# Kernel optimization log

Hardware: AMD Instinct MI355X
Metric: run time of the kernel (lower is better)

Reference implementation:

```python
import jax, jax.numpy as jnp
import numpy as np
import math

MIN_NORM = 1e-15
EPS = 1e-7
MAX_NORM = 1e6

N = 100000      # num nodes (aaa)
E = 1600000     # num edges
D_IN = 129      # embedding_num (1 time coord + 128 spatial)
D_OUT = 128     # output1_dim
MAXLEN = 50
B = 4096
NCLASS = 5

# ---------------- Hyperboloid manifold ops (HGCN-style) ----------------

def proj(x, c):
    K = 1. / c
    y = x[..., 1:]
    y_sq = jnp.sum(y * y, axis=-1, keepdims=True)
    x0 = jnp.sqrt(jnp.clip(K + y_sq, EPS))
    return jnp.concatenate([x0, y], axis=-1)

def proj_tan0(u, c):
    # zero out the time coordinate
    return jnp.concatenate([jnp.zeros_like(u[..., :1]), u[..., 1:]], axis=-1)

def expmap0(u, c):
    K = 1. / c
    sqrtK = jnp.sqrt(K)
    x = u[..., 1:]
    xn = jnp.maximum(jnp.linalg.norm(x, axis=-1, keepdims=True), MIN_NORM)
    theta = xn / sqrtK
    first = sqrtK * jnp.cosh(theta)
    rest = sqrtK * jnp.sinh(theta) * x / xn
    return proj(jnp.concatenate([first, rest], axis=-1), c)

def logmap0(x, c):
    K = 1. / c
    sqrtK = jnp.sqrt(K)
    y = x[..., 1:]
    yn = jnp.maximum(jnp.linalg.norm(y, axis=-1, keepdims=True), MIN_NORM)
    theta = jnp.clip(x[..., 0:1] / sqrtK, 1.0 + EPS)
    rest = sqrtK * jnp.arccosh(theta) * y / yn
    return jnp.concatenate([jnp.zeros_like(theta), rest], axis=-1)

def minkowski_dot(x, y):
    return jnp.sum(x * y, axis=-1, keepdims=True) - 2.0 * x[..., 0:1] * y[..., 0:1]

def minkowski_norm(u):
    return jnp.sqrt(jnp.clip(minkowski_dot(u, u), EPS))

def expmap(u, x, c):
    K = 1. / c
    sqrtK = jnp.sqrt(K)
    normu = jnp.minimum(minkowski_norm(u), MAX_NORM)
    theta = jnp.maximum(normu / sqrtK, MIN_NORM)
    result = jnp.cosh(theta) * x + jnp.sinh(theta) * u / theta
    return proj(result, c)

def proj_tan(u, x, c):
    ux = jnp.sum(x[..., 1:] * u[..., 1:], axis=-1, keepdims=True)
    vals0 = ux / jnp.clip(x[..., 0:1], EPS)
    return jnp.concatenate([vals0, u[..., 1:]], axis=-1)

def ptransp0(x, u, c):
    K = 1. / c
    sqrtK = jnp.sqrt(K)
    x0 = x[..., 0:1]
    y = x[..., 1:]
    yn = jnp.maximum(jnp.linalg.norm(y, axis=-1, keepdims=True), MIN_NORM)
    yhat = y / yn
    v = jnp.concatenate([-yn, (sqrtK - x0) * yhat], axis=-1)
    alpha = jnp.sum(yhat * u[..., 1:], axis=-1, keepdims=True) / sqrtK
    return proj_tan(u - alpha * v, x, c)

def mobius_add(x, y, c):
    u = logmap0(y, c)
    v = ptransp0(x, jnp.broadcast_to(u, x.shape), c)
    return expmap(v, x, c)

def mobius_add0(x, y, c):
    # tangent-space addition at the origin
    return expmap0(logmap0(x, c) + logmap0(y, c), c)

def mobius_matvec1(m, x, c):
    return expmap0(logmap0(x, c) @ m, c)

def mobius_matvec0(n, x, c):
    # per-row scalar mobius scaling (n is (N,1))
    return expmap0(n * logmap0(x, c), c)

def hyp_bias_point(b, c):
    return proj(expmap0(proj_tan0(b[None, :], c), c), c)

def gcn_layer(x, w, b, rows, cols, vals, c, n_nodes):
    out = mobius_matvec1(w, x, c)
    out = mobius_add(out, hyp_bias_point(b, c), c)
    out = logmap0(out, c)
    out = jax.ops.segment_sum(vals[:, None] * out[cols], rows, num_segments=n_nodes)
    return proj(expmap0(out, c), c)


def setup_inputs() -> dict:
    key = jax.random.key(0)
    ks = jax.random.split(key, 20)
    def ku(k, shape, fan_in):
        bound = 1.0 / math.sqrt(fan_in)
        return jax.random.uniform(k, shape, jnp.float32, -bound, bound)
    inp = {}
    inp['A1_tensor'] = jax.random.normal(ks[0], (N, D_IN), jnp.float32)
    inp['adj_rows'] = jax.random.randint(ks[1], (E,), 0, N)
    inp['adj_cols'] = jax.random.randint(ks[2], (E,), 0, N)
    inp['adj_vals'] = jax.random.uniform(ks[3], (E,), jnp.float32) * 0.1
    inp['batch_idx'] = jax.random.randint(ks[4], (B, 1, MAXLEN), 0, N)
    inp['raw_c'] = jnp.array([math.log(math.exp(1.0) - 1.0)], jnp.float32)
    inp['n_param'] = jax.random.uniform(ks[5], (N, 1), jnp.float32)
    inp['Lin1'] = ku(ks[6], (D_IN, D_OUT), D_IN)
    inp['Lin1_bias'] = ku(ks[7], (D_OUT,), D_IN)
    inp['gc1_w'] = ku(ks[8], (D_IN, D_OUT), D_IN)
    inp['gc1_b'] = ku(ks[9], (D_OUT,), D_IN)
    inp['gc2_w'] = ku(ks[10], (D_OUT, D_OUT), D_OUT)
    inp['gc2_b'] = ku(ks[11], (D_OUT,), D_OUT)
    inp['weight'] = ku(ks[12], (D_OUT, MAXLEN), D_OUT)
    inp['weight2'] = ku(ks[13], (D_OUT, MAXLEN), D_OUT)
    inp['conv1_w'] = ku(ks[14], (MAXLEN,), MAXLEN)
    inp['conv1_b'] = ku(ks[15], (1,), MAXLEN)
    inp['conv2_w'] = ku(ks[16], (MAXLEN,), MAXLEN)
    inp['conv2_b'] = ku(ks[17], (1,), MAXLEN)
    inp['classifier'] = ku(ks[18], (2 * MAXLEN, NCLASS), 2 * MAXLEN)
    inp['classifier_bias'] = ku(ks[19], (NCLASS,), 2 * MAXLEN)
    return inp


def reference(A1_tensor, adj_rows, adj_cols, adj_vals, batch_idx, raw_c, n_param,
              Lin1, Lin1_bias, gc1_w, gc1_b, gc2_w, gc2_b, weight, weight2,
              conv1_w, conv1_b, conv2_w, conv2_b, classifier, classifier_bias):
    c = jax.nn.softplus(raw_c)[0] + 1e-5
    bi = batch_idx[:, 0, :]                       # (B, L)
    flat = bi.reshape(-1)

    x_tan = proj_tan0(A1_tensor, c)
    a = proj(expmap0(x_tan, c), c)                # (N, D_IN)

    a1 = mobius_matvec1(Lin1, a, c)               # (N, D_OUT)
    a1 = mobius_add(a1, hyp_bias_point(Lin1_bias, c), c)
    a2 = mobius_matvec0(n_param, a1, c)

    x_1 = gcn_layer(a, gc1_w, gc1_b, adj_rows, adj_cols, adj_vals, c, N)
    x_1 = mobius_matvec0(1.0 - n_param, x_1, c)
    x_1 = mobius_add0(x_1, a2, c)
    x_2 = gcn_layer(x_1, gc2_w, gc2_b, adj_rows, adj_cols, adj_vals, c, N)

    # readout branch 1: x_2 gathered on batch indices
    s2 = logmap0(x_2[flat].reshape(bi.shape[0], bi.shape[1], D_OUT), c)  # (B,L,D)
    s2 = jnp.einsum('bld,dt->blt', s2, weight)    # (B, L, MAXLEN)
    s2 = jnp.einsum('blt,l->bt', s2, conv1_w) + conv1_b  # kernel-size-1 conv over channels

    # readout branch 2: a1 gathered on batch indices
    s3 = logmap0(a1[flat].reshape(bi.shape[0], bi.shape[1], D_OUT), c)
    s3 = jnp.einsum('bld,dt->blt', s3, weight2)
    s3 = jnp.einsum('blt,l->bt', s3, conv2_w) + conv2_b

    sel = jnp.concatenate([s2, s3], axis=1)       # (B, 2*MAXLEN)
    pre = sel @ classifier + classifier_bias      # (B, NCLASS)
    return jnp.argmax(pre, axis=-1), sel
```

## Files before the change

kernel.cpp:

```cpp
#include <hip/hip_runtime.h>
#include <math.h>


__device__ __forceinline__ float wsum(float x){
  x += __shfl_xor(x, 32);
  x += __shfl_xor(x, 16);
  x += __shfl_xor(x, 8);
  x += __shfl_xor(x, 4);
  x += __shfl_xor(x, 2);
  x += __shfl_xor(x, 1);
  return x;
}

__device__ __forceinline__ void get_c(const float* rc, float& K, float& sK){
  float c = log1pf(expf(rc[0])) + 1e-5f;
  K  = 1.0f / c;
  sK = sqrtf(K);
}

__device__ __forceinline__ float sinhx_over_x(float x){
  if (x > 1e-3f){
    float e  = __expf(x);
    float em = __builtin_amdgcn_rcpf(e);
    return 0.5f*(e - em) * __builtin_amdgcn_rcpf(x);
  }
  return 1.0f + x*x*(1.0f/6.0f);
}

__device__ __forceinline__ float facosh(float x){
  return __logf(x + sqrtf(fmaxf(fmaf(x, x, -1.0f), 0.0f)));
}

__device__ __forceinline__ unsigned int pack_bf16(float x, float y){
  unsigned int bx = __float_as_uint(x);
  unsigned int by = __float_as_uint(y);
  bx = (bx + 0x7fffu + ((bx >> 16) & 1u)) >> 16;
  by = (by + 0x7fffu + ((by >> 16) & 1u)) & 0xffff0000u;
  return bx | by;
}
__device__ __forceinline__ float bf_lo(unsigned int p){ return __uint_as_float(p << 16); }
__device__ __forceinline__ float bf_hi(unsigned int p){ return __uint_as_float(p & 0xffff0000u); }

__device__ __forceinline__ void chain_scalars(float tt, float tu, float uu,
                                              float K, float sK,
                                              float& At, float& Au){
  float xn  = fmaxf(sqrtf(tt), 1e-15f);
  float th  = xn / sK;
  float f   = sinhx_over_x(th);
  float pn2 = f*f*tt;
  float p0  = sqrtf(fmaxf(K + pn2, 1e-7f));
  float S_yu = f * tu;
  float yn  = fmaxf(sqrtf(pn2), 1e-15f);
  float inv_yn = __builtin_amdgcn_rcpf(yn);
  float alpha = S_yu * inv_yn / sK;
  float coef  = alpha * (sK - p0);
  float cy  = coef * inv_yn;
  float cyf = cy * f;
  float pdw  = S_yu - cy*pn2;
  float spsq = uu - 2.f*cy*S_yu + cy*cy*pn2;
  float w0 = pdw / fmaxf(p0, 1e-7f);
  float md = spsq - w0*w0;
  float normu = fminf(sqrtf(fmaxf(md, 1e-7f)), 1e6f);
  float th2 = fmaxf(normu / sK, 1e-15f);
  float e  = __expf(th2);
  float em = __builtin_amdgcn_rcpf(e);
  float ch = 0.5f*(e + em);
  float g  = (th2 > 1e-3f) ? 0.5f*(e - em)*__builtin_amdgcn_rcpf(th2)
                           : 1.0f + th2*th2*(1.0f/6.0f);
  float rn2 = ch*ch*pn2 + 2.f*ch*g*pdw + g*g*spsq;
  float r0 = sqrtf(fmaxf(K + rn2, 1e-7f));
  float ynf = fmaxf(sqrtf(rn2), 1e-15f);
  float thf = fmaxf(r0/sK, 1.f+1e-7f);
  float rf = sK * facosh(thf) * __builtin_amdgcn_rcpf(ynf);
  At = rf*(ch*f - g*cyf);
  Au = rf*g;
}

__global__ __launch_bounds__(256) void stage_a(const float* __restrict__ A1,
                                               float* __restrict__ L,
                                               int* __restrict__ cnt,
                                               const float* __restrict__ b0,
                                               const float* __restrict__ b1,
                                               const float* __restrict__ b2,
                                               float* __restrict__ uu3, int n){
  size_t i = (size_t)blockIdx.x * 256 + threadIdx.x;
  size_t total = (size_t)n * 128;
  if (i < total){
    size_t row = i >> 7; int j = (int)(i & 127);
    L[i] = A1[row*129 + 1 + j];
  }
  if (i < (size_t)n) cnt[i] = 0;
  if (blockIdx.x == 0 && threadIdx.x < 64){
    int lane = threadIdx.x;
    const float* bs[3] = {b0, b1, b2};
    for (int k = 0; k < 3; ++k){
      float x = lane ? bs[k][2*lane] : 0.0f;
      float y = bs[k][2*lane+1];
      float s = wsum(x*x + y*y);
      if (lane == 0) uu3[k] = s;
    }
  }
}

__global__ __launch_bounds__(256) void gemm_chain(const float* __restrict__ A,
                                                  const float* __restrict__ W,
                                                  const float* __restrict__ bias,
                                                  const float* __restrict__ uu3, int uuidx,
                                                  const float* __restrict__ raw_c,
                                                  float* __restrict__ outF,
                                                  unsigned int* __restrict__ outH,
                                                  int mode, int nrows){
  __shared__ float As[16][132];
  __shared__ float Ws[16][132];
  int tid = threadIdx.x;
  int r0  = blockIdx.x * 128;
  int tx  = tid & 15, ty = tid >> 4;
  float4 aA[2], aW[2];
  int rowA[2], kqA[2], kW[2], cqW[2];
  #pragma unroll
  for (int t = 0; t < 2; ++t){
    int f = tid + t*256;
    rowA[t] = f >> 2; kqA[t] = f & 3;
    kW[t]   = f >> 5; cqW[t] = f & 31;
  }

  auto loadA = [&](int kc){
    #pragma unroll
    for (int t = 0; t < 2; ++t){
      int rg = r0 + rowA[t];
      aA[t] = make_float4(0.f,0.f,0.f,0.f);
      if (rg < nrows) aA[t] = *(const float4*)&A[(size_t)rg*128 + kc*16 + kqA[t]*4];
    }
  };
  auto loadW = [&](int kc){
    #pragma unroll
    for (int t = 0; t < 2; ++t)
      aW[t] = *(const float4*)&W[(size_t)(kc*16 + kW[t])*128 + cqW[t]*4];
  };

  float acc[8][8];
  #pragma unroll
  for (int i = 0; i < 8; ++i)
    #pragma unroll
    for (int j = 0; j < 8; ++j) acc[i][j] = 0.f;

  loadA(0); loadW(0);
  for (int kc = 0; kc < 8; ++kc){
    __syncthreads();
    #pragma unroll
    for (int t = 0; t < 2; ++t){
      As[kqA[t]*4+0][rowA[t]] = aA[t].x;
      As[kqA[t]*4+1][rowA[t]] = aA[t].y;
      As[kqA[t]*4+2][rowA[t]] = aA[t].z;
      As[kqA[t]*4+3][rowA[t]] = aA[t].w;
      *(float4*)&Ws[kW[t]][cqW[t]*4] = aW[t];
    }
    __syncthreads();
    if (kc < 7){ loadA(kc+1); loadW(kc+1); }
    #pragma unroll
    for (int k = 0; k < 16; ++k){
      float4 a0 = *(const float4*)&As[k][ty*8];
      float4 a1 = *(const float4*)&As[k][ty*8+4];
      float4 w0 = *(const float4*)&Ws[k][tx*8];
      float4 w1 = *(const float4*)&Ws[k][tx*8+4];
      float av[8] = {a0.x,a0.y,a0.z,a0.w,a1.x,a1.y,a1.z,a1.w};
      float wv[8] = {w0.x,w0.y,w0.z,w0.w,w1.x,w1.y,w1.z,w1.w};
      #pragma unroll
      for (int i = 0; i < 8; ++i)
        #pragma unroll
        for (int j = 0; j < 8; ++j)
          acc[i][j] = fmaf(av[i], wv[j], acc[i][j]);
    }
  }

  float K, sK; get_c(raw_c, K, sK);
  float uu = uu3[uuidx];
  float uv[8];
  #pragma unroll
  for (int j = 0; j < 8; ++j){
    int col = tx*8 + j;
    uv[j] = (col == 0) ? 0.f : bias[col];
  }
  if (tx == 0){
    #pragma unroll
    for (int i = 0; i < 8; ++i) acc[i][0] = 0.f;
  }
  #pragma unroll
  for (int i = 0; i < 8; ++i){
    float tt = 0.f, tu = 0.f;
    #pragma unroll
    for (int j = 0; j < 8; ++j){
      tt = fmaf(acc[i][j], acc[i][j], tt);
      tu = fmaf(acc[i][j], uv[j], tu);
    }
    #pragma unroll
    for (int m = 1; m <= 8; m <<= 1){
      tt += __shfl_xor(tt, m);
      tu += __shfl_xor(tu, m);
    }
    float At, Au; chain_scalars(tt, tu, uu, K, sK, At, Au);
    int rg = r0 + ty*8 + i;
    if (rg < nrows){
      float o[8];
      #pragma unroll
      for (int j = 0; j < 8; ++j) o[j] = fmaf(At, acc[i][j], Au*uv[j]);
      if (mode == 0){
        *(float4*)&outF[(size_t)rg*128 + tx*8]     = make_float4(o[0],o[1],o[2],o[3]);
        *(float4*)&outF[(size_t)rg*128 + tx*8 + 4] = make_float4(o[4],o[5],o[6],o[7]);
      } else {
        uint4 pk;
        pk.x = pack_bf16(o[0], o[1]);
        pk.y = pack_bf16(o[2], o[3]);
        pk.z = pack_bf16(o[4], o[5]);
        pk.w = pack_bf16(o[6], o[7]);
        *(uint4*)&outH[(size_t)rg*64 + tx*4] = pk;
      }
    }
  }
}

__global__ __launch_bounds__(256) void hist_k(const int* __restrict__ rows,
                                              int* __restrict__ cnt,
                                              int* __restrict__ rnk, int e){
  int base = (blockIdx.x * 256 + threadIdx.x) * 4;
  if (base + 3 < e){
    int4 r = *(const int4*)&rows[base];
    int k0 = atomicAdd(&cnt[r.x], 1);
    int k1 = atomicAdd(&cnt[r.y], 1);
    int k2 = atomicAdd(&cnt[r.z], 1);
    int k3 = atomicAdd(&cnt[r.w], 1);
    *(int4*)&rnk[base] = make_int4(k0, k1, k2, k3);
  } else {
    for (int i = base; i < e; ++i) rnk[i] = atomicAdd(&cnt[rows[i]], 1);
  }
}

#define SCAN_ITEMS 4
__global__ __launch_bounds__(256) void scan1(const int* __restrict__ cnt,
                                             int* __restrict__ off,
                                             int* __restrict__ bsum, int n){
  __shared__ int sh[256];
  int tid = threadIdx.x;
  int base = blockIdx.x * 256 * SCAN_ITEMS + tid * SCAN_ITEMS;
  int v[SCAN_ITEMS]; int s = 0;
  #pragma unroll
  for (int i = 0; i < SCAN_ITEMS; ++i){ int idx = base+i; v[i] = (idx < n) ? cnt[idx] : 0; s += v[i]; }
  sh[tid] = s; __syncthreads();
  for (int o = 1; o < 256; o <<= 1){
    int t = (tid >= o) ? sh[tid - o] : 0; __syncthreads();
    sh[tid] += t; __syncthreads();
  }
  int excl = sh[tid] - s;
  if (tid == 255) bsum[blockIdx.x] = sh[tid];
  int run = excl;
  #pragma unroll
  for (int i = 0; i < SCAN_ITEMS; ++i){ int idx = base+i; if (idx < n) off[idx] = run; run += v[i]; }
}

__global__ void scan2(int* bsum, int G){
  if (threadIdx.x == 0 && blockIdx.x == 0){
    int run = 0;
    for (int i = 0; i < G; ++i){ int t = bsum[i]; bsum[i] = run; run += t; }
  }
}

__global__ void scan3(int* __restrict__ off, const int* __restrict__ bsum, int n){
  int i = blockIdx.x * blockDim.x + threadIdx.x;
  if (i < n) off[i] += bsum[i / (256*SCAN_ITEMS)];
}

__global__ __launch_bounds__(256) void fill_k(const int* __restrict__ rows,
                                              const int* __restrict__ cols,
                                              const float* __restrict__ vals,
                                              const int* __restrict__ off,
                                              const int* __restrict__ rnk,
                                              int2* __restrict__ ecv, int e){
  int base = (blockIdx.x * 256 + threadIdx.x) * 4;
  if (base + 3 < e){
    int4   r = *(const int4*)&rows[base];
    int4   q = *(const int4*)&rnk[base];
    int4   c = *(const int4*)&cols[base];
    float4 v = *(const float4*)&vals[base];
    int o0 = off[r.x], o1 = off[r.y], o2 = off[r.z], o3 = off[r.w];
    ecv[o0 + q.x] = make_int2(c.x, __float_as_int(v.x));
    ecv[o1 + q.y] = make_int2(c.y, __float_as_int(v.y));
    ecv[o2 + q.z] = make_int2(c.z, __float_as_int(v.z));
    ecv[o3 + q.w] = make_int2(c.w, __float_as_int(v.w));
  } else {
    for (int i = base; i < e; ++i)
      ecv[off[rows[i]] + rnk[i]] = make_int2(cols[i], __float_as_int(vals[i]));
  }
}

__device__ __forceinline__ float2 seg_gather_bf16(const unsigned int* __restrict__ h,
                                                  const int* __restrict__ off,
                                                  const int* __restrict__ cnt,
                                                  const int2* __restrict__ ecv,
                                                  int row, int lane){
  float ax = 0.f, ay = 0.f, bx = 0.f, by = 0.f;
  int st = off[row], deg = cnt[row];
  const unsigned int* __restrict__ hb = h + lane;
  for (int b = 0; b < deg; b += 64){
    int k = b + lane;
    int cc = 0; float vv = 0.f;
    if (k < deg){ int2 e = ecv[st+k]; cc = e.x; vv = __int_as_float(e.y); }
    int m = min(64, deg - b);
    for (int j = 0; j < m; j += 8){
      int   c0=__shfl(cc,j+0), c1=__shfl(cc,j+1), c2=__shfl(cc,j+2), c3=__shfl(cc,j+3);
      int   c4=__shfl(cc,j+4), c5=__shfl(cc,j+5), c6=__shfl(cc,j+6), c7=__shfl(cc,j+7);
      float v0=__shfl(vv,j+0), v1=__shfl(vv,j+1), v2=__shfl(vv,j+2), v3=__shfl(vv,j+3);
      float v4=__shfl(vv,j+4), v5=__shfl(vv,j+5), v6=__shfl(vv,j+6), v7=__shfl(vv,j+7);
      unsigned int p0 = hb[(size_t)c0*64];
      unsigned int p1 = hb[(size_t)c1*64];
      unsigned int p2 = hb[(size_t)c2*64];
      unsigned int p3 = hb[(size_t)c3*64];
      unsigned int p4 = hb[(size_t)c4*64];
      unsigned int p5 = hb[(size_t)c5*64];
      unsigned int p6 = hb[(size_t)c6*64];
      unsigned int p7 = hb[(size_t)c7*64];
      ax = fmaf(v0, bf_lo(p0), ax); ay = fmaf(v0, bf_hi(p0), ay);
      bx = fmaf(v1, bf_lo(p1), bx); by = fmaf(v1, bf_hi(p1), by);
      ax = fmaf(v2, bf_lo(p2), ax); ay = fmaf(v2, bf_hi(p2), ay);
      bx = fmaf(v3, bf_lo(p3), bx); by = fmaf(v3, bf_hi(p3), by);
      ax = fmaf(v4, bf_lo(p4), ax); ay = fmaf(v4, bf_hi(p4), ay);
      bx = fmaf(v5, bf_lo(p5), bx); by = fmaf(v5, bf_hi(p5), by);
      ax = fmaf(v6, bf_lo(p6), ax); ay = fmaf(v6, bf_hi(p6), ay);
      bx = fmaf(v7, bf_lo(p7), bx); by = fmaf(v7, bf_hi(p7), by);
    }
  }
  return make_float2(ax + bx, ay + by);
}

__global__ __launch_bounds__(256) void seg_x1(const unsigned int* __restrict__ h1,
                                              const int* __restrict__ off,
                                              const int* __restrict__ cnt,
                                              const int2* __restrict__ ecv,
                                              const float* __restrict__ loga1,
                                              const float* __restrict__ nparam,
                                              float* __restrict__ Lx1, int n){
  int row  = (int)((blockIdx.x * blockDim.x + threadIdx.x) >> 6);
  int lane = threadIdx.x & 63;
  if (row >= n) return;
  float2 acc = seg_gather_bf16(h1, off, cnt, ecv, row, lane);
  float nv = nparam[row];
  float2 la1 = *(const float2*)&loga1[(size_t)row*128 + 2*lane];
  float ox = (1.f-nv)*acc.x + nv*la1.x;
  float oy = (1.f-nv)*acc.y + nv*la1.y;
  *(float2*)&Lx1[(size_t)row*128 + 2*lane] = make_float2(ox, oy);
}

__global__ __launch_bounds__(256) void seg_x2(const unsigned int* __restrict__ h2,
                                              const int* __restrict__ off,
                                              const int* __restrict__ cnt,
                                              const int2* __restrict__ ecv,
                                              float* __restrict__ Lx2, int n){
  int row  = (int)((blockIdx.x * blockDim.x + threadIdx.x) >> 6);
  int lane = threadIdx.x & 63;
  if (row >= n) return;
  float2 acc = seg_gather_bf16(h2, off, cnt, ecv, row, lane);
  *(float2*)&Lx2[(size_t)row*128 + 2*lane] = acc;
}

__global__ __launch_bounds__(128) void batch_head(const float* __restrict__ Lx2,
                                                  const float* __restrict__ loga1,
                                                  const int* __restrict__ bidx,
                                                  const float* __restrict__ weight,
                                                  const float* __restrict__ weight2,
                                                  const float* __restrict__ c1w,
                                                  const float* __restrict__ c1b,
                                                  const float* __restrict__ c2w,
                                                  const float* __restrict__ c2b,
                                                  const float* __restrict__ cls,
                                                  const float* __restrict__ clsb,
                                                  float* __restrict__ out, int Bn){
  __shared__ float sg2[128], sg3[128], ssel[100], spre[5];
  __shared__ int sbi[50];
  __shared__ float sc1[50], sc2[50];
  int b = blockIdx.x, d = threadIdx.x;
  const int* bi = bidx + (size_t)b * 50;
  if (d < 50){ sbi[d] = bi[d]; sc1[d] = c1w[d]; sc2[d] = c2w[d]; }
  __syncthreads();
  int lane = d & 63;
  bool lo = d < 64;
  const float* __restrict__ tab = lo ? Lx2 : loga1;
  const float* __restrict__ cw = lo ? sc1 : sc2;
  float gx = 0.f, gy = 0.f;
  const float2* __restrict__ t2 = (const float2*)tab + lane;
  #pragma unroll
  for (int l = 0; l < 50; l += 5){
    int i0 = sbi[l+0], i1 = sbi[l+1], i2 = sbi[l+2], i3 = sbi[l+3], i4 = sbi[l+4];
    float2 p0 = t2[(size_t)i0*64];
    float2 p1 = t2[(size_t)i1*64];
    float2 p2 = t2[(size_t)i2*64];
    float2 p3 = t2[(size_t)i3*64];
    float2 p4 = t2[(size_t)i4*64];
    float w0 = cw[l+0], w1 = cw[l+1], w2 = cw[l+2], w3 = cw[l+3], w4 = cw[l+4];
    gx = fmaf(w0, p0.x, gx); gy = fmaf(w0, p0.y, gy);
    gx = fmaf(w1, p1.x, gx); gy = fmaf(w1, p1.y, gy);
    gx = fmaf(w2, p2.x, gx); gy = fmaf(w2, p2.y, gy);
    gx = fmaf(w3, p3.x, gx); gy = fmaf(w3, p3.y, gy);
    gx = fmaf(w4, p4.x, gx); gy = fmaf(w4, p4.y, gy);
  }
  if (lo){ sg2[2*lane] = gx; sg2[2*lane+1] = gy; }
  else   { sg3[2*lane] = gx; sg3[2*lane+1] = gy; }
  __syncthreads();
  if (d < 50){
    float s = 0.f;
    for (int k = 0; k < 128; ++k) s = fmaf(sg2[k], weight[k*50 + d], s);
    s += c1b[0];
    ssel[d] = s;
    out[(size_t)Bn + (size_t)b*100 + d] = s;
  } else if (d >= 64 && d < 114){
    int t = d - 64;
    float s = 0.f;
    for (int k = 0; k < 128; ++k) s = fmaf(sg3[k], weight2[k*50 + t], s);
    s += c2b[0];
    ssel[50 + t] = s;
    out[(size_t)Bn + (size_t)b*100 + 50 + t] = s;
  }
  __syncthreads();
  if (d < 5){
    float s = clsb[d];
    for (int j = 0; j < 100; ++j) s = fmaf(ssel[j], cls[j*5 + d], s);
    spre[d] = s;
  }
  __syncthreads();
  if (d == 0){
    int best = 0; float bv = spre[0];
    #pragma unroll
    for (int k = 1; k < 5; ++k) if (spre[k] > bv){ bv = spre[k]; best = k; }
    out[b] = (float)best;
  }
}

extern "C" void kernel_launch(void* const* d_in, const int* in_sizes, int n_in,
                              void* d_out, int out_size, void* d_ws, size_t ws_size,
                              hipStream_t stream) {
  const float* A1     = (const float*)d_in[0];
  const int*   rows   = (const int*)  d_in[1];
  const int*   cols   = (const int*)  d_in[2];
  const float* vals   = (const float*)d_in[3];
  const int*   bidx   = (const int*)  d_in[4];
  const float* raw_c  = (const float*)d_in[5];
  const float* nparam = (const float*)d_in[6];
  const float* Lin1   = (const float*)d_in[7];
  const float* Lin1_b = (const float*)d_in[8];
  const float* gc1_w  = (const float*)d_in[9];
  const float* gc1_b  = (const float*)d_in[10];
  const float* gc2_w  = (const float*)d_in[11];
  const float* gc2_b  = (const float*)d_in[12];
  const float* weight = (const float*)d_in[13];
  const float* weight2= (const float*)d_in[14];
  const float* c1w    = (const float*)d_in[15];
  const float* c1b    = (const float*)d_in[16];
  const float* c2w    = (const float*)d_in[17];
  const float* c2b    = (const float*)d_in[18];
  const float* cls    = (const float*)d_in[19];
  const float* clsb   = (const float*)d_in[20];

  int N  = in_sizes[0] / 129;
  int E  = in_sizes[1];
  int Bn = in_sizes[4] / 50;
  size_t NF = (size_t)N * 128;

  float* S0 = (float*)d_ws;
  float* S1 = S0 + NF;
  float* S3 = S1 + NF;
  unsigned int* Hb = (unsigned int*)(S3 + NF);
  int* cnt    = (int*)(Hb + NF/2);
  int* off    = cnt + N;
  int* rnk    = off + N;
  int* bsum   = rnk + E;
  int2* ecv   = (int2*)(bsum + 4096);
  float* uu3  = (float*)(ecv + E);

  int rowBlocks  = (N + 3) / 4;
  int gemmBlocks = (N + 127) / 128;
  int G = (N + 256*SCAN_ITEMS - 1) / (256*SCAN_ITEMS);
  int eBlocks4 = (E/4 + 255) / 256 + 1;

  stage_a<<<(int)((NF + 255)/256), 256, 0, stream>>>(A1, S0, cnt, Lin1_b, gc1_b, gc2_b, uu3, N);

  hist_k<<<eBlocks4, 256, 0, stream>>>(rows, cnt, rnk, E);
  scan1<<<G, 256, 0, stream>>>(cnt, off, bsum, N);
  scan2<<<1, 64, 0, stream>>>(bsum, G);
  scan3<<<(N+255)/256, 256, 0, stream>>>(off, bsum, N);
  fill_k<<<eBlocks4, 256, 0, stream>>>(rows, cols, vals, off, rnk, ecv, E);

  gemm_chain<<<gemmBlocks, 256, 0, stream>>>(S0, Lin1 + 128, Lin1_b, uu3, 0, raw_c,
                                             S3, (unsigned int*)nullptr, 0, N);
  gemm_chain<<<gemmBlocks, 256, 0, stream>>>(S0, gc1_w + 128, gc1_b, uu3, 1, raw_c,
                                             (float*)nullptr, Hb, 1, N);
  seg_x1<<<rowBlocks, 256, 0, stream>>>(Hb, off, cnt, ecv, S3, nparam, S1, N);
  gemm_chain<<<gemmBlocks, 256, 0, stream>>>(S1, gc2_w, gc2_b, uu3, 2, raw_c,
                                             (float*)nullptr, Hb, 1, N);
  seg_x2<<<rowBlocks, 256, 0, stream>>>(Hb, off, cnt, ecv, S0, N);
  batch_head<<<Bn, 128, 0, stream>>>(S0, S3, bidx, weight, weight2, c1w, c1b,
                                     c2w, c2b, cls, clsb, (float*)d_out, Bn);
}
```

Baseline: 668.6 us.

## Fuse the two GEMMs sharing input S0 and move to 512-thread blocks

The Lin1 and gc1 GEMMs both read S0, so they are merged into one kernel that loads each A tile once and accumulates against both weight matrices. Both outputs (fp32 for Lin1, bf16 for gc1) are written from the same epilogue. Both GEMM kernels now use 512 threads per 128-row tile with a 4x8 per-thread micro-tile instead of 8x8, which halves per-thread accumulators and raises parallelism. The fused kernel carries 64 accumulators per thread plus a third shared-memory tile, so register pressure and occupancy are the main risk.

New measurement: 663.4 us. About the same (-0.8%).

```diff
diff --git a/kernel.cpp b/kernel.cpp
--- a/kernel.cpp
+++ b/kernel.cpp
@@ -102,71 +102,170 @@
   }
 }
 
-__global__ __launch_bounds__(256) void gemm_chain(const float* __restrict__ A,
+__global__ __launch_bounds__(512) void gemm_chain2(const float* __restrict__ A,
+                                                   const float* __restrict__ W1,
+                                                   const float* __restrict__ W2,
+                                                   const float* __restrict__ b1,
+                                                   const float* __restrict__ b2,
+                                                   const float* __restrict__ uu3,
+                                                   const float* __restrict__ raw_c,
+                                                   float* __restrict__ outF,
+                                                   unsigned int* __restrict__ outH,
+                                                   int nrows){
+  __shared__ float As[16][132];
+  __shared__ float W1s[16][132];
+  __shared__ float W2s[16][132];
+  int tid = threadIdx.x;
+  int r0  = blockIdx.x * 128;
+  int tx  = tid & 15, ty = tid >> 4;
+  int rowA = tid >> 2, kqA = tid & 3;
+  int kW   = tid >> 5, cqW = tid & 31;
+  float4 aA, aW1, aW2;
+
+  auto loadT = [&](int kc){
+    int rg = r0 + rowA;
+    aA = make_float4(0.f,0.f,0.f,0.f);
+    if (rg < nrows) aA = *(const float4*)&A[(size_t)rg*128 + kc*16 + kqA*4];
+    aW1 = *(const float4*)&W1[(size_t)(kc*16 + kW)*128 + cqW*4];
+    aW2 = *(const float4*)&W2[(size_t)(kc*16 + kW)*128 + cqW*4];
+  };
+
+  float acc1[4][8], acc2[4][8];
+  #pragma unroll
+  for (int i = 0; i < 4; ++i)
+    #pragma unroll
+    for (int j = 0; j < 8; ++j){ acc1[i][j] = 0.f; acc2[i][j] = 0.f; }
+
+  loadT(0);
+  for (int kc = 0; kc < 8; ++kc){
+    __syncthreads();
+    As[kqA*4+0][rowA] = aA.x;
+    As[kqA*4+1][rowA] = aA.y;
+    As[kqA*4+2][rowA] = aA.z;
+    As[kqA*4+3][rowA] = aA.w;
+    *(float4*)&W1s[kW][cqW*4] = aW1;
+    *(float4*)&W2s[kW][cqW*4] = aW2;
+    __syncthreads();
+    if (kc < 7) loadT(kc+1);
+    #pragma unroll
+    for (int k = 0; k < 16; ++k){
+      float4 a  = *(const float4*)&As[k][ty*4];
+      float4 p0 = *(const float4*)&W1s[k][tx*8];
+      float4 p1 = *(const float4*)&W1s[k][tx*8+4];
+      float4 q0 = *(const float4*)&W2s[k][tx*8];
+      float4 q1 = *(const float4*)&W2s[k][tx*8+4];
+      float av[4] = {a.x,a.y,a.z,a.w};
+      float wv1[8] = {p0.x,p0.y,p0.z,p0.w,p1.x,p1.y,p1.z,p1.w};
+      float wv2[8] = {q0.x,q0.y,q0.z,q0.w,q1.x,q1.y,q1.z,q1.w};
+      #pragma unroll
+      for (int i = 0; i < 4; ++i)
+        #pragma unroll
+        for (int j = 0; j < 8; ++j){
+          acc1[i][j] = fmaf(av[i], wv1[j], acc1[i][j]);
+          acc2[i][j] = fmaf(av[i], wv2[j], acc2[i][j]);
+        }
+    }
+  }
+
+  float K, sK; get_c(raw_c, K, sK);
+  float uuA = uu3[0], uuB = uu3[1];
+  float uv1[8], uv2[8];
+  #pragma unroll
+  for (int j = 0; j < 8; ++j){
+    int col = tx*8 + j;
+    uv1[j] = (col == 0) ? 0.f : b1[col];
+    uv2[j] = (col == 0) ? 0.f : b2[col];
+  }
+  if (tx == 0){
+    #pragma unroll
+    for (int i = 0; i < 4; ++i){ acc1[i][0] = 0.f; acc2[i][0] = 0.f; }
+  }
+  #pragma unroll
+  for (int i = 0; i < 4; ++i){
+    float t1 = 0.f, u1 = 0.f, t2 = 0.f, u2 = 0.f;
+    #pragma unroll
+    for (int j = 0; j < 8; ++j){
+      t1 = fmaf(acc1[i][j], acc1[i][j], t1);
+      u1 = fmaf(acc1[i][j], uv1[j], u1);
+      t2 = fmaf(acc2[i][j], acc2[i][j], t2);
+      u2 = fmaf(acc2[i][j], uv2[j], u2);
+    }
+    #pragma unroll
+    for (int m = 1; m <= 8; m <<= 1){
+      t1 += __shfl_xor(t1, m); u1 += __shfl_xor(u1, m);
+      t2 += __shfl_xor(t2, m); u2 += __shfl_xor(u2, m);
+    }
+    float At1, Au1, At2, Au2;
+    chain_scalars(t1, u1, uuA, K, sK, At1, Au1);
+    chain_scalars(t2, u2, uuB, K, sK, At2, Au2);
+    int rg = r0 + ty*4 + i;
+    if (rg < nrows){
+      float o1[8], o2[8];
+      #pragma unroll
+      for (int j = 0; j < 8; ++j){
+        o1[j] = fmaf(At1, acc1[i][j], Au1*uv1[j]);
+        o2[j] = fmaf(At2, acc2[i][j], Au2*uv2[j]);
+      }
+      *(float4*)&outF[(size_t)rg*128 + tx*8]     = make_float4(o1[0],o1[1],o1[2],o1[3]);
+      *(float4*)&outF[(size_t)rg*128 + tx*8 + 4] = make_float4(o1[4],o1[5],o1[6],o1[7]);
+      uint4 pk;
+      pk.x = pack_bf16(o2[0], o2[1]);
+      pk.y = pack_bf16(o2[2], o2[3]);
+      pk.z = pack_bf16(o2[4], o2[5]);
+      pk.w = pack_bf16(o2[6], o2[7]);
+      *(uint4*)&outH[(size_t)rg*64 + tx*4] = pk;
+    }
+  }
+}
+
+__global__ __launch_bounds__(512) void gemm_chain(const float* __restrict__ A,
                                                   const float* __restrict__ W,
                                                   const float* __restrict__ bias,
                                                   const float* __restrict__ uu3, int uuidx,
                                                   const float* __restrict__ raw_c,
-                                                  float* __restrict__ outF,
                                                   unsigned int* __restrict__ outH,
-                                                  int mode, int nrows){
+                                                  int nrows){
   __shared__ float As[16][132];
   __shared__ float Ws[16][132];
   int tid = threadIdx.x;
   int r0  = blockIdx.x * 128;
   int tx  = tid & 15, ty = tid >> 4;
-  float4 aA[2], aW[2];
-  int rowA[2], kqA[2], kW[2], cqW[2];
-  #pragma unroll
-  for (int t = 0; t < 2; ++t){
-    int f = tid + t*256;
-    rowA[t] = f >> 2; kqA[t] = f & 3;
-    kW[t]   = f >> 5; cqW[t] = f & 31;
-  }
-
-  auto loadA = [&](int kc){
-    #pragma unroll
-    for (int t = 0; t < 2; ++t){
-      int rg = r0 + rowA[t];
-      aA[t] = make_float4(0.f,0.f,0.f,0.f);
-      if (rg < nrows) aA[t] = *(const float4*)&A[(size_t)rg*128 + kc*16 + kqA[t]*4];
-    }
+  int rowA = tid >> 2, kqA = tid & 3;
+  int kW   = tid >> 5, cqW = tid & 31;
+  float4 aA, aW;
+
+  auto loadT = [&](int kc){
+    int rg = r0 + rowA;
+    aA = make_float4(0.f,0.f,0.f,0.f);
+    if (rg < nrows) aA = *(const float4*)&A[(size_t)rg*128 + kc*16 + kqA*4];
+    aW = *(const float4*)&W[(size_t)(kc*16 + kW)*128 + cqW*4];
   };
-  auto loadW = [&](int kc){
-    #pragma unroll
-    for (int t = 0; t < 2; ++t)
-      aW[t] = *(const float4*)&W[(size_t)(kc*16 + kW[t])*128 + cqW[t]*4];
-  };
-
-  float acc[8][8];
-  #pragma unroll
-  for (int i = 0; i < 8; ++i)
+
+  float acc[4][8];
+  #pragma unroll
+  for (int i = 0; i < 4; ++i)
     #pragma unroll
     for (int j = 0; j < 8; ++j) acc[i][j] = 0.f;
 
-  loadA(0); loadW(0);
+  loadT(0);
   for (int kc = 0; kc < 8; ++kc){
     __syncthreads();
-    #pragma unroll
-    for (int t = 0; t < 2; ++t){
-      As[kqA[t]*4+0][rowA[t]] = aA[t].x;
-      As[kqA[t]*4+1][rowA[t]] = aA[t].y;
-      As[kqA[t]*4+2][rowA[t]] = aA[t].z;
-      As[kqA[t]*4+3][rowA[t]] = aA[t].w;
-      *(float4*)&Ws[kW[t]][cqW[t]*4] = aW[t];
-    }
+    As[kqA*4+0][rowA] = aA.x;
+    As[kqA*4+1][rowA] = aA.y;
+    As[kqA*4+2][rowA] = aA.z;
+    As[kqA*4+3][rowA] = aA.w;
+    *(float4*)&Ws[kW][cqW*4] = aW;
     __syncthreads();
-    if (kc < 7){ loadA(kc+1); loadW(kc+1); }
+    if (kc < 7) loadT(kc+1);
     #pragma unroll
     for (int k = 0; k < 16; ++k){
-      float4 a0 = *(const float4*)&As[k][ty*8];
-      float4 a1 = *(const float4*)&As[k][ty*8+4];
+      float4 a  = *(const float4*)&As[k][ty*4];
       float4 w0 = *(const float4*)&Ws[k][tx*8];
       float4 w1 = *(const float4*)&Ws[k][tx*8+4];
-      float av[8] = {a0.x,a0.y,a0.z,a0.w,a1.x,a1.y,a1.z,a1.w};
+      float av[4] = {a.x,a.y,a.z,a.w};
       float wv[8] = {w0.x,w0.y,w0.z,w0.w,w1.x,w1.y,w1.z,w1.w};
       #pragma unroll
-      for (int i = 0; i < 8; ++i)
+      for (int i = 0; i < 4; ++i)
         #pragma unroll
         for (int j = 0; j < 8; ++j)
           acc[i][j] = fmaf(av[i], wv[j], acc[i][j]);
@@ -183,10 +282,10 @@
   }
   if (tx == 0){
     #pragma unroll
-    for (int i = 0; i < 8; ++i) acc[i][0] = 0.f;
-  }
-  #pragma unroll
-  for (int i = 0; i < 8; ++i){
+    for (int i = 0; i < 4; ++i) acc[i][0] = 0.f;
+  }
+  #pragma unroll
+  for (int i = 0; i < 4; ++i){
     float tt = 0.f, tu = 0.f;
     #pragma unroll
     for (int j = 0; j < 8; ++j){
@@ -199,22 +298,17 @@
       tu += __shfl_xor(tu, m);
     }
     float At, Au; chain_scalars(tt, tu, uu, K, sK, At, Au);
-    int rg = r0 + ty*8 + i;
+    int rg = r0 + ty*4 + i;
     if (rg < nrows){
       float o[8];
       #pragma unroll
       for (int j = 0; j < 8; ++j) o[j] = fmaf(At, acc[i][j], Au*uv[j]);
-      if (mode == 0){
-        *(float4*)&outF[(size_t)rg*128 + tx*8]     = make_float4(o[0],o[1],o[2],o[3]);
-        *(float4*)&outF[(size_t)rg*128 + tx*8 + 4] = make_float4(o[4],o[5],o[6],o[7]);
-      } else {
-        uint4 pk;
-        pk.x = pack_bf16(o[0], o[1]);
-        pk.y = pack_bf16(o[2], o[3]);
-        pk.z = pack_bf16(o[4], o[5]);
-        pk.w = pack_bf16(o[6], o[7]);
-        *(uint4*)&outH[(size_t)rg*64 + tx*4] = pk;
-      }
+      uint4 pk;
+      pk.x = pack_bf16(o[0], o[1]);
+      pk.y = pack_bf16(o[2], o[3]);
+      pk.z = pack_bf16(o[4], o[5]);
+      pk.w = pack_bf16(o[6], o[7]);
+      *(uint4*)&outH[(size_t)rg*64 + tx*4] = pk;
     }
   }
 }
@@ -487,13 +581,10 @@
   scan3<<<(N+255)/256, 256, 0, stream>>>(off, bsum, N);
   fill_k<<<eBlocks4, 256, 0, stream>>>(rows, cols, vals, off, rnk, ecv, E);
 
-  gemm_chain<<<gemmBlocks, 256, 0, stream>>>(S0, Lin1 + 128, Lin1_b, uu3, 0, raw_c,
-                                             S3, (unsigned int*)nullptr, 0, N);
-  gemm_chain<<<gemmBlocks, 256, 0, stream>>>(S0, gc1_w + 128, gc1_b, uu3, 1, raw_c,
-                                             (float*)nullptr, Hb, 1, N);
+  gemm_chain2<<<gemmBlocks, 512, 0, stream>>>(S0, Lin1 + 128, gc1_w + 128,
+                                              Lin1_b, gc1_b, uu3, raw_c, S3, Hb, N);
   seg_x1<<<rowBlocks, 256, 0, stream>>>(Hb, off, cnt, ecv, S3, nparam, S1, N);
-  gemm_chain<<<gemmBlocks, 256, 0, stream>>>(S1, gc2_w, gc2_b, uu3, 2, raw_c,
-                                             (float*)nullptr, Hb, 1, N);
+  gemm_chain<<<gemmBlocks, 512, 0, stream>>>(S1, gc2_w, gc2_b, uu3, 2, raw_c, Hb, N);
   seg_x2<<<rowBlocks, 256, 0, stream>>>(Hb, off, cnt, ecv, S0, N);
   batch_head<<<Bn, 128, 0, stream>>>(S0, S3, bidx, weight, weight2, c1w, c1b,
                                      c2w, c2b, cls, clsb, (float*)d_out, Bn);
```

## Replace FP32 SIMT GEMMs with split-bf16 MFMA GEMMs fused with the hyperbolic chain

Applied to the files above, without the earlier changes.

The three N×128×128 FP32 shared-memory GEMMs become matrix-core kernels that split each operand into a bf16 high and low part and issue three MFMA products (hi*hi, hi*lo, lo*hi) to approximate FP32 accuracy. The input embedding and the seg_x1 output are now written directly as hi/lo bf16 pairs, and the weights are split and transposed by a new small kernel. The A tile stays in registers and the weights are read straight from global memory without LDS. This removes the FP32 FMA-bound inner loop at the cost of extra split passes, a slight accuracy loss, and narrower output stores.

Result: no change. 656.9 us (-1.7%).

```diff
diff --git a/kernel.cpp b/kernel.cpp
--- a/kernel.cpp
+++ b/kernel.cpp
@@ -1,6 +1,10 @@
 #include <hip/hip_runtime.h>
 #include <math.h>
 
+
+typedef unsigned short ushort_t;
+typedef __attribute__((ext_vector_type(8))) short short8;
+typedef __attribute__((ext_vector_type(4))) float f32x4;
 
 __device__ __forceinline__ float wsum(float x){
   x += __shfl_xor(x, 32);
@@ -31,6 +35,14 @@
   return __logf(x + sqrtf(fmaxf(fmaf(x, x, -1.0f), 0.0f)));
 }
 
+__device__ __forceinline__ ushort_t bf16_rne(float x){
+  unsigned int u = __float_as_uint(x);
+  u += 0x7fffu + ((u >> 16) & 1u);
+  return (ushort_t)(u >> 16);
+}
+__device__ __forceinline__ float bf2f(ushort_t h){
+  return __uint_as_float(((unsigned int)h) << 16);
+}
 __device__ __forceinline__ unsigned int pack_bf16(float x, float y){
   unsigned int bx = __float_as_uint(x);
   unsigned int by = __float_as_uint(y);
@@ -77,7 +89,8 @@
 }
 
 __global__ __launch_bounds__(256) void stage_a(const float* __restrict__ A1,
-                                               float* __restrict__ L,
+                                               ushort_t* __restrict__ Lhi,
+                                               ushort_t* __restrict__ Llo,
                                                int* __restrict__ cnt,
                                                const float* __restrict__ b0,
                                                const float* __restrict__ b1,
@@ -87,7 +100,10 @@
   size_t total = (size_t)n * 128;
   if (i < total){
     size_t row = i >> 7; int j = (int)(i & 127);
-    L[i] = A1[row*129 + 1 + j];
+    float v = A1[row*129 + 1 + j];
+    ushort_t h = bf16_rne(v);
+    Lhi[i] = h;
+    Llo[i] = bf16_rne(v - bf2f(h));
   }
   if (i < (size_t)n) cnt[i] = 0;
   if (blockIdx.x == 0 && threadIdx.x < 64){
@@ -102,74 +118,56 @@
   }
 }
 
-__global__ __launch_bounds__(256) void gemm_chain(const float* __restrict__ A,
-                                                  const float* __restrict__ W,
+__global__ __launch_bounds__(256) void split_w(const float* __restrict__ W,
+                                               ushort_t* __restrict__ Whi,
+                                               ushort_t* __restrict__ Wlo){
+  int id = blockIdx.x * 256 + threadIdx.x;
+  int k = id >> 7, nn = id & 127;
+  float v = W[(size_t)k*128 + nn];
+  ushort_t h = bf16_rne(v);
+  Whi[(size_t)nn*128 + k] = h;
+  Wlo[(size_t)nn*128 + k] = bf16_rne(v - bf2f(h));
+}
+
+__global__ __launch_bounds__(256) void mfma_chain(const ushort_t* __restrict__ Ahi,
+                                                  const ushort_t* __restrict__ Alo,
+                                                  const ushort_t* __restrict__ Whi,
+                                                  const ushort_t* __restrict__ Wlo,
                                                   const float* __restrict__ bias,
                                                   const float* __restrict__ uu3, int uuidx,
                                                   const float* __restrict__ raw_c,
                                                   float* __restrict__ outF,
                                                   unsigned int* __restrict__ outH,
-                                                  int mode, int nrows){
-  __shared__ float As[16][132];
-  __shared__ float Ws[16][132];
-  int tid = threadIdx.x;
-  int r0  = blockIdx.x * 128;
-  int tx  = tid & 15, ty = tid >> 4;
-  float4 aA[2], aW[2];
-  int rowA[2], kqA[2], kW[2], cqW[2];
-  #pragma unroll
-  for (int t = 0; t < 2; ++t){
-    int f = tid + t*256;
-    rowA[t] = f >> 2; kqA[t] = f & 3;
-    kW[t]   = f >> 5; cqW[t] = f & 31;
-  }
-
-  auto loadA = [&](int kc){
+                                                  int mode, int n){
+  int wave = blockIdx.x * 4 + (threadIdx.x >> 6);
+  int m0 = wave * 16;
+  if (m0 >= n) return;
+  int lane = threadIdx.x & 63;
+  int c = lane & 15, quad = lane >> 4;
+
+  int ra = m0 + c; if (ra > n - 1) ra = n - 1;
+  short8 ahi[4], alo[4];
+  #pragma unroll
+  for (int kc = 0; kc < 4; ++kc){
+    size_t aoff = (size_t)ra*128 + kc*32 + quad*8;
+    ahi[kc] = *(const short8*)&Ahi[aoff];
+    alo[kc] = *(const short8*)&Alo[aoff];
+  }
+
+  f32x4 acc[8];
+  #pragma unroll
+  for (int t = 0; t < 8; ++t){
+    f32x4 z = {0.f, 0.f, 0.f, 0.f};
+    acc[t] = z;
+    size_t wrow = (size_t)(t*16 + c) * 128;
     #pragma unroll
-    for (int t = 0; t < 2; ++t){
-      int rg = r0 + rowA[t];
-      aA[t] = make_float4(0.f,0.f,0.f,0.f);
-      if (rg < nrows) aA[t] = *(const float4*)&A[(size_t)rg*128 + kc*16 + kqA[t]*4];
-    }
-  };
-  auto loadW = [&](int kc){
-    #pragma unroll
-    for (int t = 0; t < 2; ++t)
-      aW[t] = *(const float4*)&W[(size_t)(kc*16 + kW[t])*128 + cqW[t]*4];
-  };
-
-  float acc[8][8];
-  #pragma unroll
-  for (int i = 0; i < 8; ++i)
-    #pragma unroll
-    for (int j = 0; j < 8; ++j) acc[i][j] = 0.f;
-
-  loadA(0); loadW(0);
-  for (int kc = 0; kc < 8; ++kc){
-    __syncthreads();
-    #pragma unroll
-    for (int t = 0; t < 2; ++t){
-      As[kqA[t]*4+0][rowA[t]] = aA[t].x;
-      As[kqA[t]*4+1][rowA[t]] = aA[t].y;
-      As[kqA[t]*4+2][rowA[t]] = aA[t].z;
-      As[kqA[t]*4+3][rowA[t]] = aA[t].w;
-      *(float4*)&Ws[kW[t]][cqW[t]*4] = aW[t];
-    }
-    __syncthreads();
-    if (kc < 7){ loadA(kc+1); loadW(kc+1); }
-    #pragma unroll
-    for (int k = 0; k < 16; ++k){
-      float4 a0 = *(const float4*)&As[k][ty*8];
-      float4 a1 = *(const float4*)&As[k][ty*8+4];
-      float4 w0 = *(const float4*)&Ws[k][tx*8];
-      float4 w1 = *(const float4*)&Ws[k][tx*8+4];
-      float av[8] = {a0.x,a0.y,a0.z,a0.w,a1.x,a1.y,a1.z,a1.w};
-      float wv[8] = {w0.x,w0.y,w0.z,w0.w,w1.x,w1.y,w1.z,w1.w};
-      #pragma unroll
-      for (int i = 0; i < 8; ++i)
-        #pragma unroll
-        for (int j = 0; j < 8; ++j)
-          acc[i][j] = fmaf(av[i], wv[j], acc[i][j]);
+    for (int kc = 0; kc < 4; ++kc){
+      size_t woff = wrow + kc*32 + quad*8;
+      short8 bhi = *(const short8*)&Whi[woff];
+      short8 blo = *(const short8*)&Wlo[woff];
+      acc[t] = __builtin_amdgcn_mfma_f32_16x16x32_bf16(ahi[kc], bhi, acc[t], 0, 0, 0);
+      acc[t] = __builtin_amdgcn_mfma_f32_16x16x32_bf16(ahi[kc], blo, acc[t], 0, 0, 0);
+      acc[t] = __builtin_amdgcn_mfma_f32_16x16x32_bf16(alo[kc], bhi, acc[t], 0, 0, 0);
     }
   }
 
@@ -177,21 +175,22 @@
   float uu = uu3[uuidx];
   float uv[8];
   #pragma unroll
-  for (int j = 0; j < 8; ++j){
-    int col = tx*8 + j;
-    uv[j] = (col == 0) ? 0.f : bias[col];
-  }
-  if (tx == 0){
-    #pragma unroll
-    for (int i = 0; i < 8; ++i) acc[i][0] = 0.f;
-  }
-  #pragma unroll
-  for (int i = 0; i < 8; ++i){
+  for (int t = 0; t < 8; ++t){
+    int col = t*16 + c;
+    uv[t] = (col == 0) ? 0.f : bias[col];
+  }
+  if (c == 0){
+    f32x4 z = {0.f, 0.f, 0.f, 0.f};
+    acc[0] = z;
+  }
+  #pragma unroll
+  for (int r = 0; r < 4; ++r){
     float tt = 0.f, tu = 0.f;
     #pragma unroll
-    for (int j = 0; j < 8; ++j){
-      tt = fmaf(acc[i][j], acc[i][j], tt);
-      tu = fmaf(acc[i][j], uv[j], tu);
+    for (int t = 0; t < 8; ++t){
+      float v = acc[t][r];
+      tt = fmaf(v, v, tt);
+      tu = fmaf(v, uv[t], tu);
     }
     #pragma unroll
     for (int m = 1; m <= 8; m <<= 1){
@@ -199,22 +198,26 @@
       tu += __shfl_xor(tu, m);
     }
     float At, Au; chain_scalars(tt, tu, uu, K, sK, At, Au);
-    int rg = r0 + ty*8 + i;
-    if (rg < nrows){
-      float o[8];
+    int row = m0 + quad*4 + r;
+    if (row < n){
+      if (mode == 0){
+        #pragma unroll
+        for (int t = 0; t < 8; ++t){
+          float o = fmaf(At, acc[t][r], Au*uv[t]);
+          outF[(size_t)row*128 + t*16 + c] = o;
+        }
+      } else {
+        #pragma unroll
+        for (int t = 0; t < 8; ++t){
+          float o  = fmaf(At, acc[t][r], Au*uv[t]);
+          float on = __shfl_xor(o, 1);
+          if (!(c & 1))
+            outH[(size_t)row*64 + t*8 + (c >> 1)] = pack_bf16(o, on);
+        }
+      }
+    } else {
       #pragma unroll
-      for (int j = 0; j < 8; ++j) o[j] = fmaf(At, acc[i][j], Au*uv[j]);
-      if (mode == 0){
-        *(float4*)&outF[(size_t)rg*128 + tx*8]     = make_float4(o[0],o[1],o[2],o[3]);
-        *(float4*)&outF[(size_t)rg*128 + tx*8 + 4] = make_float4(o[4],o[5],o[6],o[7]);
-      } else {
-        uint4 pk;
-        pk.x = pack_bf16(o[0], o[1]);
-        pk.y = pack_bf16(o[2], o[3]);
-        pk.z = pack_bf16(o[4], o[5]);
-        pk.w = pack_bf16(o[6], o[7]);
-        *(uint4*)&outH[(size_t)rg*64 + tx*4] = pk;
-      }
+      for (int t = 0; t < 8; ++t){ float o = 0.f; (void)__shfl_xor(o, 1); }
     }
   }
 }
@@ -337,7 +340,8 @@
                                               const int2* __restrict__ ecv,
                                               const float* __restrict__ loga1,
                                               const float* __restrict__ nparam,
-                                              float* __restrict__ Lx1, int n){
+                                              unsigned int* __restrict__ X1hi,
+                                              unsigned int* __restrict__ X1lo, int n){
   int row  = (int)((blockIdx.x * blockDim.x + threadIdx.x) >> 6);
   int lane = threadIdx.x & 63;
   if (row >= n) return;
@@ -346,7 +350,9 @@
   float2 la1 = *(const float2*)&loga1[(size_t)row*128 + 2*lane];
   float ox = (1.f-nv)*acc.x + nv*la1.x;
   float oy = (1.f-nv)*acc.y + nv*la1.y;
-  *(float2*)&Lx1[(size_t)row*128 + 2*lane] = make_float2(ox, oy);
+  unsigned int hp = pack_bf16(ox, oy);
+  X1hi[(size_t)row*64 + lane] = hp;
+  X1lo[(size_t)row*64 + lane] = pack_bf16(ox - bf_lo(hp), oy - bf_hi(hp));
 }
 
 __global__ __launch_bounds__(256) void seg_x2(const unsigned int* __restrict__ h2,
@@ -463,11 +469,18 @@
   int Bn = in_sizes[4] / 50;
   size_t NF = (size_t)N * 128;
 
-  float* S0 = (float*)d_ws;
-  float* S1 = S0 + NF;
-  float* S3 = S1 + NF;
-  unsigned int* Hb = (unsigned int*)(S3 + NF);
-  int* cnt    = (int*)(Hb + NF/2);
+  ushort_t* Lhi = (ushort_t*)d_ws;
+  ushort_t* Llo = Lhi + NF;
+  float*    S0  = (float*)d_ws;
+  float*    S3  = (float*)(Llo + NF);
+  unsigned int* Hb   = (unsigned int*)(S3 + NF);
+  unsigned int* X1hi = Hb + NF/2;
+  unsigned int* X1lo = X1hi + NF/2;
+  ushort_t* Wb = (ushort_t*)(X1lo + NF/2);
+  ushort_t* W1h = Wb,           *W1l = Wb + 16384;
+  ushort_t* W2h = Wb + 2*16384, *W2l = Wb + 3*16384;
+  ushort_t* W3h = Wb + 4*16384, *W3l = Wb + 5*16384;
+  int* cnt    = (int*)(Wb + 6*16384);
   int* off    = cnt + N;
   int* rnk    = off + N;
   int* bsum   = rnk + E;
@@ -475,11 +488,16 @@
   float* uu3  = (float*)(ecv + E);
 
   int rowBlocks  = (N + 3) / 4;
-  int gemmBlocks = (N + 127) / 128;
+  int strips     = (N + 15) / 16;
+  int mBlocks    = (strips + 3) / 4;
   int G = (N + 256*SCAN_ITEMS - 1) / (256*SCAN_ITEMS);
   int eBlocks4 = (E/4 + 255) / 256 + 1;
 
-  stage_a<<<(int)((NF + 255)/256), 256, 0, stream>>>(A1, S0, cnt, Lin1_b, gc1_b, gc2_b, uu3, N);
+  stage_a<<<(int)((NF + 255)/256), 256, 0, stream>>>(A1, Lhi, Llo, cnt,
+                                                     Lin1_b, gc1_b, gc2_b, uu3, N);
+  split_w<<<64, 256, 0, stream>>>(Lin1 + 128, W1h, W1l);
+  split_w<<<64, 256, 0, stream>>>(gc1_w + 128, W2h, W2l);
+  split_w<<<64, 256, 0, stream>>>(gc2_w, W3h, W3l);
 
   hist_k<<<eBlocks4, 256, 0, stream>>>(rows, cnt, rnk, E);
   scan1<<<G, 256, 0, stream>>>(cnt, off, bsum, N);
@@ -487,13 +505,14 @@
   scan3<<<(N+255)/256, 256, 0, stream>>>(off, bsum, N);
   fill_k<<<eBlocks4, 256, 0, stream>>>(rows, cols, vals, off, rnk, ecv, E);
 
-  gemm_chain<<<gemmBlocks, 256, 0, stream>>>(S0, Lin1 + 128, Lin1_b, uu3, 0, raw_c,
-                                             S3, (unsigned int*)nullptr, 0, N);
-  gemm_chain<<<gemmBlocks, 256, 0, stream>>>(S0, gc1_w + 128, gc1_b, uu3, 1, raw_c,
-                                             (float*)nullptr, Hb, 1, N);
-  seg_x1<<<rowBlocks, 256, 0, stream>>>(Hb, off, cnt, ecv, S3, nparam, S1, N);
-  gemm_chain<<<gemmBlocks, 256, 0, stream>>>(S1, gc2_w, gc2_b, uu3, 2, raw_c,
-                                             (float*)nullptr, Hb, 1, N);
+  mfma_chain<<<mBlocks, 256, 0, stream>>>(Lhi, Llo, W1h, W1l, Lin1_b, uu3, 0, raw_c,
+                                          S3, (unsigned int*)nullptr, 0, N);
+  mfma_chain<<<mBlocks, 256, 0, stream>>>(Lhi, Llo, W2h, W2l, gc1_b, uu3, 1, raw_c,
+                                          (float*)nullptr, Hb, 1, N);
+  seg_x1<<<rowBlocks, 256, 0, stream>>>(Hb, off, cnt, ecv, S3, nparam, X1hi, X1lo, N);
+  mfma_chain<<<mBlocks, 256, 0, stream>>>((const ushort_t*)X1hi, (const ushort_t*)X1lo,
+                                          W3h, W3l, gc2_b, uu3, 2, raw_c,
+                                          (float*)nullptr, Hb, 1, N);
   seg_x2<<<rowBlocks, 256, 0, stream>>>(Hb, off, cnt, ecv, S0, N);
   batch_head<<<Bn, 128, 0, stream>>>(S0, S3, bidx, weight, weight2, c1w, c1b,
                                      c2w, c2b, cls, clsb, (float*)d_out, Bn);
```
